# Performance work log

Hardware: AMD Instinct MI355X
Metric: run time of the kernel (lower is better)

## Reference

```python
import jax, jax.numpy as jnp
import numpy as np

DIM = 512
QK_DIM = 128
HIDDEN = 1024


def setup_inputs() -> dict:
    key = jax.random.key(0)
    ks = jax.random.split(key, 8)
    b, n = 4, 4096
    x = jax.random.normal(ks[0], (b, n, DIM), dtype=jnp.float32)
    # nn.Linear(dim, hidden*2)
    w_hidden = jax.random.normal(ks[1], (DIM, 2 * HIDDEN), dtype=jnp.float32) / np.sqrt(DIM)
    b_hidden = jnp.zeros((2 * HIDDEN,), dtype=jnp.float32)
    # nn.Linear(dim, qk_dim, bias=False)
    w_qk = jax.random.normal(ks[2], (DIM, QK_DIM), dtype=jnp.float32) / np.sqrt(DIM)
    # OffsetScale params (gamma init 1, beta init 0; randomize slightly for a nontrivial test)
    q_gamma = 1.0 + 0.02 * jax.random.normal(ks[3], (QK_DIM,), dtype=jnp.float32)
    q_beta = 0.02 * jax.random.normal(ks[4], (QK_DIM,), dtype=jnp.float32)
    k_gamma = 1.0 + 0.02 * jax.random.normal(ks[5], (QK_DIM,), dtype=jnp.float32)
    k_beta = 0.02 * jax.random.normal(ks[6], (QK_DIM,), dtype=jnp.float32)
    # nn.Linear(hidden, dim)
    w_out = jax.random.normal(ks[7], (HIDDEN, DIM), dtype=jnp.float32) / np.sqrt(HIDDEN)
    b_out = jnp.zeros((DIM,), dtype=jnp.float32)
    return {
        "x": x,
        "w_hidden": w_hidden, "b_hidden": b_hidden,
        "w_qk": w_qk,
        "q_gamma": q_gamma, "q_beta": q_beta,
        "k_gamma": k_gamma, "k_beta": k_beta,
        "w_out": w_out, "b_out": b_out,
    }


def reference(x, w_hidden, b_hidden, w_qk, q_gamma, q_beta, k_gamma, k_beta, w_out, b_out):
    scale = QK_DIM ** -0.5
    # to_hidden -> chunk into v, gate (NOTE: source applies no activation here)
    hid = jnp.einsum('bnd,dh->bnh', x, w_hidden) + b_hidden  # [b, n, 2*hidden]
    v, gate = jnp.split(hid, 2, axis=-1)                     # each [b, n, hidden]
    qk = jnp.einsum('bnd,de->bne', x, w_qk)                  # [b, n, qk_dim]
    q = qk * q_gamma + q_beta
    k = qk * k_gamma + k_beta
    sim = jnp.einsum('bid,bjd->bij', q, k) * scale           # [b, n, n]
    attn = jnp.square(jax.nn.relu(sim))                      # ReLU^2, no softmax
    out = jnp.einsum('bij,bjh->bih', attn, v)                # [b, n, hidden]
    out = out * gate
    out = jnp.einsum('bnh,hd->bnd', out, w_out) + b_out      # [b, n, dim]
    return out + x  # add_residual=True
```

## Files before the change

### kernel.cpp

```cpp
#include <hip/hip_runtime.h>
#include <hip/hip_bf16.h>

typedef __attribute__((ext_vector_type(8))) short bf16x8;
typedef __attribute__((ext_vector_type(4))) float f32x4;
typedef unsigned short u16;

__device__ __forceinline__ u16 f2b(float f) {
  __hip_bfloat16 h = __float2bfloat16(f);
  return __builtin_bit_cast(unsigned short, h);
}
__device__ __forceinline__ float b2f(u16 u) {
  __hip_bfloat16 h = __builtin_bit_cast(__hip_bfloat16, u);
  return __bfloat162float(h);
}

#define BAR() __builtin_amdgcn_s_barrier()
#define LGKM0() do { asm volatile("s_waitcnt lgkmcnt(0)" ::: "memory"); __builtin_amdgcn_sched_barrier(0); } while (0)
#define LGKM4() do { asm volatile("s_waitcnt lgkmcnt(4)" ::: "memory"); __builtin_amdgcn_sched_barrier(0); } while (0)
#define LGKM8() do { asm volatile("s_waitcnt lgkmcnt(8)" ::: "memory"); __builtin_amdgcn_sched_barrier(0); } while (0)
#define VMCNT4() asm volatile("s_waitcnt vmcnt(4)" ::: "memory")
#define VMCNT2() asm volatile("s_waitcnt vmcnt(2)" ::: "memory")
#define VMCNT0() asm volatile("s_waitcnt vmcnt(0)" ::: "memory")

#define EPI_HID 0
#define EPI_QK 1
#define EPI_PV 3
#define EPI_OUT 4

__device__ __forceinline__ void stage_tile(char* sbase, const char* gbase, int ld_bytes, int tid) {
#pragma unroll
  for (int i = 0; i < 4; ++i) {
    int o = (i * 256 + tid) * 16;
    int row = o >> 7;
    int cb = o & 127;
    int scb = cb ^ ((row & 7) << 4);
    const char* src = gbase + (long)row * ld_bytes + scb;
    __builtin_amdgcn_global_load_lds((const __attribute__((address_space(1))) void*)src,
                                     (__attribute__((address_space(3))) void*)(sbase + o),
                                     16, 0, 0);
  }
}

template <int EPI>
__global__ __launch_bounds__(256, 2) void gemm_tn(
    const char* Ab, const char* Bb, long sAbat, long sBbat,
    int lda_b, int ldb_b, int nkt,
    u16* o0, u16* o1,
    const float* a0, const float* a1, const float* a2, const float* a3,
    float* fout, const float* xres) {
  __shared__ __align__(16) char lds[32768];
  char* sA = lds;
  char* sB = lds + 16384;
  const int tid = threadIdx.x;
  const int lane = tid & 63;
  const int wave = tid >> 6;
  const int wm = wave >> 1, wn = wave & 1;
  const int l16 = lane & 15, lq = lane >> 4;
  const int bat = blockIdx.z;
  const int row0 = blockIdx.y * 128;
  const int col0 = blockIdx.x * 128;

  const char* Abase = Ab + (long)bat * sAbat + (long)row0 * lda_b;
  const char* Bbase = Bb + (long)bat * sBbat + (long)col0 * ldb_b;

  f32x4 acc[4][4];
#pragma unroll
  for (int i = 0; i < 4; ++i)
#pragma unroll
    for (int j = 0; j < 4; ++j) acc[i][j] = (f32x4){0.f, 0.f, 0.f, 0.f};

  for (int kt = 0; kt < nkt; ++kt) {
    stage_tile(sA, Abase + (long)kt * 128, lda_b, tid);
    stage_tile(sB, Bbase + (long)kt * 128, ldb_b, tid);
    __syncthreads();
#pragma unroll
    for (int kk = 0; kk < 2; ++kk) {
      bf16x8 af[4], bfr[4];
#pragma unroll
      for (int mf = 0; mf < 4; ++mf) {
        int r = wm * 64 + mf * 16 + l16;
        int kb = kk * 64 + lq * 16;
        af[mf] = *(const bf16x8*)(sA + r * 128 + (kb ^ ((r & 7) << 4)));
      }
#pragma unroll
      for (int nf = 0; nf < 4; ++nf) {
        int r = wn * 64 + nf * 16 + l16;
        int kb = kk * 64 + lq * 16;
        bfr[nf] = *(const bf16x8*)(sB + r * 128 + (kb ^ ((r & 7) << 4)));
      }
#pragma unroll
      for (int mf = 0; mf < 4; ++mf)
#pragma unroll
        for (int nf = 0; nf < 4; ++nf)
          acc[mf][nf] = __builtin_amdgcn_mfma_f32_16x16x32_bf16(af[mf], bfr[nf], acc[mf][nf], 0, 0, 0);
    }
    __syncthreads();
  }

#pragma unroll
  for (int mf = 0; mf < 4; ++mf) {
#pragma unroll
    for (int nf = 0; nf < 4; ++nf) {
      const int row = row0 + wm * 64 + mf * 16 + lq * 4;
      const int col = col0 + wn * 64 + nf * 16 + l16;
      f32x4 v = acc[mf][nf];
      if constexpr (EPI == EPI_QK) {
        float qg = a0[col], qbt = a1[col], kg = a2[col], kbt = a3[col];
#pragma unroll
        for (int i = 0; i < 4; ++i) {
          float t = v[i];
          o0[(size_t)(row + i) * 128 + col] = f2b(t * qg + qbt);
          o1[(size_t)(row + i) * 128 + col] = f2b(t * kg + kbt);
        }
      } else if constexpr (EPI == EPI_OUT) {
        float bias = a0[col];
#pragma unroll
        for (int i = 0; i < 4; ++i)
          fout[(size_t)(row + i) * 512 + col] = v[i] + bias + xres[(size_t)(row + i) * 512 + col];
      }
    }
  }
}

__device__ __forceinline__ void stage_half(char* sbase, const char* gbase, long ld, int tid) {
#pragma unroll
  for (int i = 0; i < 2; ++i) {
    int o = (i * 512 + tid) * 16;
    int row = o >> 7;
    int cb = o & 127;
    int scb = cb ^ ((row & 7) << 4);
    const char* src = gbase + (long)row * ld + scb;
    __builtin_amdgcn_global_load_lds((const __attribute__((address_space(1))) void*)src,
                                     (__attribute__((address_space(3))) void*)(sbase + o),
                                     16, 0, 0);
  }
}

template <int EPI>
__global__ __launch_bounds__(512, 1) void gemm256(
    const char* Ab, const char* Bb, long sAbat, long sBbat,
    long lda, long ldb, int nkt, int nx,
    u16* o0, u16* o1,
    const float* a0, float* fout, const float* xres) {
  extern __shared__ __align__(16) char lds[];
  const int tid = threadIdx.x;
  const int lane = tid & 63;
  const int wave = tid >> 6;
  const int wm = wave >> 2;
  const int wn = wave & 3;
  const int l16 = lane & 15, lq = lane >> 4;
  const int bat = blockIdx.y;

  const int nwg = gridDim.x;
  const int qq = nwg >> 3;
  const int fid = blockIdx.x;
  const int swz = (fid & 7) * qq + (fid >> 3);
  const int row0 = (swz / nx) * 256;
  const int col0 = (swz % nx) * 256;

  const char* gA = Ab + (long)bat * sAbat + (long)row0 * lda;
  const char* gB = Bb + (long)bat * sBbat + (long)col0 * ldb;

  f32x4 acc[8][4];
#pragma unroll
  for (int i = 0; i < 8; ++i)
#pragma unroll
    for (int j = 0; j < 4; ++j) acc[i][j] = (f32x4){0.f, 0.f, 0.f, 0.f};

  const int kmask = (l16 & 7) << 4;
  const int kb0 = (lq * 16) ^ kmask;
  const int kb1 = (64 + lq * 16) ^ kmask;
  const int rB = (wn & 1) * 64;

  stage_half(lds + 32768, gB, ldb, tid);
  stage_half(lds + 32768 + 16384, gB + 128 * ldb, ldb, tid);
  stage_half(lds, gA, lda, tid);
  stage_half(lds + 16384, gA + 128 * lda, lda, tid);
  if (nkt > 1) {
    stage_half(lds + 65536 + 32768, gB + 128, ldb, tid);
    stage_half(lds + 65536 + 32768 + 16384, gB + 128 * ldb + 128, ldb, tid);
    VMCNT4();
  } else {
    VMCNT0();
  }
  BAR();

  bf16x8 af0[4], af1[4], afp0[4], afp1[4], bfr0[4], bfr1[4];
  {
    const char* myA = lds + wm * 16384;
    const char* myB = lds + 32768 + (wn >> 1) * 16384;
#pragma unroll
    for (int nf = 0; nf < 4; ++nf)
      bfr0[nf] = *(const bf16x8*)(myB + (rB + nf * 16 + l16) * 128 + kb0);
#pragma unroll
    for (int mf = 0; mf < 4; ++mf)
      af0[mf] = *(const bf16x8*)(myA + (mf * 16 + l16) * 128 + kb0);
  }

  for (int t = 0; t < nkt; ++t) {
    const char* bufc = lds + (t & 1) * 65536;
    const char* bufn = lds + ((t + 1) & 1) * 65536;
    const char* myA = bufc + wm * 16384;
    const char* myB = bufc + 32768 + (wn >> 1) * 16384;
    const char* nA = bufn + wm * 16384;
    const char* nB = bufn + 32768 + (wn >> 1) * 16384;
    char* stA = (char*)bufn;
    char* stB = (char*)bufc + 32768;
    const bool sA_ok = (t + 1) < nkt;
    const bool sB_ok = (t + 2) < nkt;

#pragma unroll
    for (int nf = 0; nf < 4; ++nf)
      bfr1[nf] = *(const bf16x8*)(myB + (rB + nf * 16 + l16) * 128 + kb1);
#pragma unroll
    for (int mf = 0; mf < 4; ++mf)
      af1[mf] = *(const bf16x8*)(myA + (mf * 16 + l16) * 128 + kb1);
    if (sA_ok) stage_half(stA, gA + (long)(t + 1) * 128, lda, tid);
    LGKM8();
    __builtin_amdgcn_s_setprio(1);
#pragma unroll
    for (int mf = 0; mf < 4; ++mf)
#pragma unroll
      for (int nf = 0; nf < 4; ++nf)
        acc[mf][nf] = __builtin_amdgcn_mfma_f32_16x16x32_bf16(af0[mf], bfr0[nf], acc[mf][nf], 0, 0, 0);
    __builtin_amdgcn_s_setprio(0);

#pragma unroll
    for (int mf = 0; mf < 4; ++mf)
      afp0[mf] = *(const bf16x8*)(myA + (64 + mf * 16 + l16) * 128 + kb0);
    if (sA_ok) stage_half(stA + 16384, gA + 128 * lda + (long)(t + 1) * 128, lda, tid);
    LGKM4();
    __builtin_amdgcn_s_setprio(1);
#pragma unroll
    for (int mf = 0; mf < 4; ++mf)
#pragma unroll
      for (int nf = 0; nf < 4; ++nf)
        acc[mf][nf] = __builtin_amdgcn_mfma_f32_16x16x32_bf16(af1[mf], bfr1[nf], acc[mf][nf], 0, 0, 0);
    __builtin_amdgcn_s_setprio(0);
    BAR();

#pragma unroll
    for (int mf = 0; mf < 4; ++mf)
      afp1[mf] = *(const bf16x8*)(myA + (64 + mf * 16 + l16) * 128 + kb1);
    if (sB_ok) stage_half(stB, gB + (long)(t + 2) * 128, ldb, tid);
    LGKM4();
    __builtin_amdgcn_s_setprio(1);
#pragma unroll
    for (int mf = 0; mf < 4; ++mf)
#pragma unroll
      for (int nf = 0; nf < 4; ++nf)
        acc[4 + mf][nf] = __builtin_amdgcn_mfma_f32_16x16x32_bf16(afp0[mf], bfr0[nf], acc[4 + mf][nf], 0, 0, 0);
    __builtin_amdgcn_s_setprio(0);
    if (sA_ok) {
      if (sB_ok) { VMCNT2(); } else { VMCNT0(); }
      BAR();
    }

    if (sA_ok) {
#pragma unroll
      for (int nf = 0; nf < 4; ++nf)
        bfr0[nf] = *(const bf16x8*)(nB + (rB + nf * 16 + l16) * 128 + kb0);
#pragma unroll
      for (int mf = 0; mf < 4; ++mf)
        af0[mf] = *(const bf16x8*)(nA + (mf * 16 + l16) * 128 + kb0);
    }
    if (sB_ok) stage_half(stB + 16384, gB + 128 * ldb + (long)(t + 2) * 128, ldb, tid);
    if (sA_ok) { LGKM8(); } else { LGKM0(); }
    __builtin_amdgcn_s_setprio(1);
#pragma unroll
    for (int mf = 0; mf < 4; ++mf)
#pragma unroll
      for (int nf = 0; nf < 4; ++nf)
        acc[4 + mf][nf] = __builtin_amdgcn_mfma_f32_16x16x32_bf16(afp1[mf], bfr1[nf], acc[4 + mf][nf], 0, 0, 0);
    __builtin_amdgcn_s_setprio(0);
    BAR();
  }

#pragma unroll
  for (int mi = 0; mi < 8; ++mi) {
#pragma unroll
    for (int ni = 0; ni < 4; ++ni) {
      const int row = row0 + wm * 128 + mi * 16 + lq * 4;
      const int col = col0 + wn * 64 + ni * 16 + l16;
      f32x4 v = acc[mi][ni];
      if constexpr (EPI == EPI_HID) {
        float bias = a0[col];
        u16* dst = (col < 1024) ? (o0 + (size_t)col * 16384 + row)
                                : (o1 + (size_t)(col - 1024) * 16384 + row);
        *(ushort4*)dst = make_ushort4(f2b(v.x + bias), f2b(v.y + bias), f2b(v.z + bias), f2b(v.w + bias));
      } else if constexpr (EPI == EPI_PV) {
        const u16* gt = o1 + (size_t)col * 16384 + (size_t)bat * 4096 + row;
        ushort4 g = *(const ushort4*)gt;
        u16* dst = o0 + (size_t)bat * 4096 * 1024;
        dst[(size_t)(row + 0) * 1024 + col] = f2b(v.x * b2f(g.x));
        dst[(size_t)(row + 1) * 1024 + col] = f2b(v.y * b2f(g.y));
        dst[(size_t)(row + 2) * 1024 + col] = f2b(v.z * b2f(g.z));
        dst[(size_t)(row + 3) * 1024 + col] = f2b(v.w * b2f(g.w));
      }
    }
  }
}

__device__ __forceinline__ void stage256(char* s, const char* g, int tid) {
#pragma unroll
  for (int i = 0; i < 8; ++i) {
    int o = (i * 512 + tid) * 16;
    int row = o >> 8;
    int cb = o & 255;
    int scb = cb ^ ((row & 7) << 4);
    __builtin_amdgcn_global_load_lds((const __attribute__((address_space(1))) void*)(g + (long)row * 256 + scb),
                                     (__attribute__((address_space(3))) void*)(s + o), 16, 0, 0);
  }
}

__global__ __launch_bounds__(512, 1) void attn_lean(
    const char* Kb, const char* Qb, u16* o0, int nx) {
  extern __shared__ __align__(16) char lds[];
  const int tid = threadIdx.x;
  const int lane = tid & 63;
  const int wave = tid >> 6;
  const int wm = wave >> 2;
  const int wn = wave & 3;
  const int l16 = lane & 15, lq = lane >> 4;
  const int bat = blockIdx.y;

  const int nwg = gridDim.x;
  const int qq = nwg >> 3;
  const int fid = blockIdx.x;
  const int swz = (fid & 7) * qq + (fid >> 3);
  const int row0 = (swz / nx) * 256;
  const int col0 = (swz % nx) * 256;

  const char* gA = Kb + (size_t)bat * 4096 * 256 + (size_t)row0 * 256;
  const char* gB = Qb + (size_t)bat * 4096 * 256 + (size_t)col0 * 256;

  stage256(lds, gA, tid);
  stage256(lds + 65536, gB, tid);
  VMCNT0();
  BAR();

  const char* myA = lds + wm * 32768;
  const char* myB = lds + 65536 + (wn >> 1) * 32768;
  const int rB = (wn & 1) * 64;
  const int kmask = (l16 & 7) << 4;

  f32x4 acc[8][4];
#pragma unroll
  for (int i = 0; i < 8; ++i)
#pragma unroll
    for (int j = 0; j < 4; ++j) acc[i][j] = (f32x4){0.f, 0.f, 0.f, 0.f};

  bf16x8 aC[8], bC[4], aN[8], bN[4];

#define LOADK(A, B, kk)                                                        \
  do {                                                                         \
    const int kb_ = ((kk) * 64 + lq * 16) ^ kmask;                             \
    _Pragma("unroll") for (int mf = 0; mf < 8; ++mf)                           \
        A[mf] = *(const bf16x8*)(myA + (mf * 16 + l16) * 256 + kb_);           \
    _Pragma("unroll") for (int nf = 0; nf < 4; ++nf)                           \
        B[nf] = *(const bf16x8*)(myB + (rB + nf * 16 + l16) * 256 + kb_);      \
  } while (0)
#define MMK(A, B)                                                              \
  do {                                                                         \
    _Pragma("unroll") for (int mf = 0; mf < 8; ++mf)                           \
        _Pragma("unroll") for (int nf = 0; nf < 4; ++nf)                       \
            acc[mf][nf] =                                                      \
        __builtin_amdgcn_mfma_f32_16x16x32_bf16(A[mf], B[nf], acc[mf][nf], 0, 0, 0); \
  } while (0)

  LOADK(aC, bC, 0);
  LOADK(aN, bN, 1);
  MMK(aC, bC);
  LOADK(aC, bC, 2);
  MMK(aN, bN);
  LOADK(aN, bN, 3);
  MMK(aC, bC);
  MMK(aN, bN);
#undef LOADK
#undef MMK

  const float scale = 0.088388347648318447f;
  u16* dst = o0 + (size_t)bat * 4096 * 4096;
#pragma unroll
  for (int mi = 0; mi < 8; ++mi) {
#pragma unroll
    for (int ni = 0; ni < 4; ++ni) {
      const int row = row0 + wm * 128 + mi * 16 + lq * 4;
      const int col = col0 + wn * 64 + ni * 16 + l16;
      f32x4 v = acc[mi][ni];
      float t0 = v.x * scale; t0 = t0 > 0.f ? t0 * t0 : 0.f;
      float t1 = v.y * scale; t1 = t1 > 0.f ? t1 * t1 : 0.f;
      float t2 = v.z * scale; t2 = t2 > 0.f ? t2 * t2 : 0.f;
      float t3 = v.w * scale; t3 = t3 > 0.f ? t3 * t3 : 0.f;
      *(ushort4*)(dst + (size_t)col * 4096 + row) =
          make_ushort4(f2b(t0), f2b(t1), f2b(t2), f2b(t3));
    }
  }
}

__global__ void conv_b(const float* in, u16* out, int n) {
  int i = (blockIdx.x * blockDim.x + threadIdx.x) * 4;
  if (i >= n) return;
  float4 f = *(const float4*)(in + i);
  *(ushort4*)(out + i) = make_ushort4(f2b(f.x), f2b(f.y), f2b(f.z), f2b(f.w));
}

__global__ void transpose_lds(const float* in, u16* out, int R, int C) {
  __shared__ float t[32][33];
  const int tx = threadIdx.x & 31, ty = threadIdx.x >> 5;
  const int c0 = blockIdx.x * 32, r0 = blockIdx.y * 32;
#pragma unroll
  for (int i = 0; i < 32; i += 8)
    t[ty + i][tx] = in[(size_t)(r0 + ty + i) * C + c0 + tx];
  __syncthreads();
#pragma unroll
  for (int i = 0; i < 32; i += 8)
    out[(size_t)(c0 + ty + i) * R + r0 + tx] = f2b(t[tx][ty + i]);
}

extern "C" void kernel_launch(void* const* d_in, const int* in_sizes, int n_in,
                              void* d_out, int out_size, void* d_ws, size_t ws_size,
                              hipStream_t stream) {
  const float* x = (const float*)d_in[0];
  const float* w_hidden = (const float*)d_in[1];
  const float* b_hidden = (const float*)d_in[2];
  const float* w_qk = (const float*)d_in[3];
  const float* q_gamma = (const float*)d_in[4];
  const float* q_beta = (const float*)d_in[5];
  const float* k_gamma = (const float*)d_in[6];
  const float* k_beta = (const float*)d_in[7];
  const float* w_out = (const float*)d_in[8];
  const float* b_out = (const float*)d_in[9];
  float* out = (float*)d_out;

  char* ws = (char*)d_ws;
  size_t off = 0;
  auto alloc = [&](size_t bytes) { char* p = ws + off; off += (bytes + 255) & ~255ull; return p; };
  u16* xb     = (u16*)alloc(16384ull * 512 * 2);
  u16* wh_t   = (u16*)alloc(2048ull * 512 * 2);
  u16* wqk_t  = (u16*)alloc(128ull * 512 * 2);
  u16* wout_t = (u16*)alloc(512ull * 1024 * 2);
  u16* v_t    = (u16*)alloc(1024ull * 16384 * 2);
  u16* g_t    = (u16*)alloc(1024ull * 16384 * 2);
  u16* qb_a   = (u16*)alloc(16384ull * 128 * 2);
  u16* kb_a   = (u16*)alloc(16384ull * 128 * 2);
  u16* attnb  = (u16*)alloc(4ull * 4096 * 4096 * 2);
  u16* out1b  = (u16*)alloc(16384ull * 1024 * 2);

  (void)hipFuncSetAttribute((const void*)gemm256<EPI_HID>, hipFuncAttributeMaxDynamicSharedMemorySize, 131072);
  (void)hipFuncSetAttribute((const void*)gemm256<EPI_PV>, hipFuncAttributeMaxDynamicSharedMemorySize, 131072);
  (void)hipFuncSetAttribute((const void*)attn_lean, hipFuncAttributeMaxDynamicSharedMemorySize, 131072);

  conv_b<<<(16384 * 512 / 4 + 255) / 256, 256, 0, stream>>>(x, xb, 16384 * 512);
  transpose_lds<<<dim3(2048 / 32, 512 / 32), 256, 0, stream>>>(w_hidden, wh_t, 512, 2048);
  transpose_lds<<<dim3(128 / 32, 512 / 32), 256, 0, stream>>>(w_qk, wqk_t, 512, 128);
  transpose_lds<<<dim3(512 / 32, 1024 / 32), 256, 0, stream>>>(w_out, wout_t, 1024, 512);

  gemm256<EPI_HID><<<dim3(512, 1), 512, 131072, stream>>>(
      (const char*)xb, (const char*)wh_t, 0, 0, 1024, 1024, 8, 8,
      v_t, g_t, b_hidden, nullptr, nullptr);
  gemm_tn<EPI_QK><<<dim3(1, 128, 1), 256, 0, stream>>>(
      (const char*)xb, (const char*)wqk_t, 0, 0, 1024, 1024, 8,
      qb_a, kb_a, q_gamma, q_beta, k_gamma, k_beta, nullptr, nullptr);
  attn_lean<<<dim3(256, 4), 512, 131072, stream>>>(
      (const char*)kb_a, (const char*)qb_a, attnb, 16);
  gemm256<EPI_PV><<<dim3(64, 4), 512, 131072, stream>>>(
      (const char*)attnb, (const char*)v_t, 4096ll * 8192, 8192, 8192, 32768, 64, 4,
      out1b, g_t, nullptr, nullptr, nullptr);
  gemm_tn<EPI_OUT><<<dim3(4, 128, 1), 256, 0, stream>>>(
      (const char*)out1b, (const char*)wout_t, 0, 0, 2048, 2048, 16,
      nullptr, nullptr, b_out, nullptr, nullptr, nullptr, out, x);
}
```

Baseline: 314.7 us.

## Replace PV GEMM with 1024-thread 16-wave kernel using smaller per-wave tiles

```diff
diff --git a/kernel.cpp b/kernel.cpp
--- a/kernel.cpp
+++ b/kernel.cpp
@@ -288,15 +288,147 @@
         u16* dst = (col < 1024) ? (o0 + (size_t)col * 16384 + row)
                                 : (o1 + (size_t)(col - 1024) * 16384 + row);
         *(ushort4*)dst = make_ushort4(f2b(v.x + bias), f2b(v.y + bias), f2b(v.z + bias), f2b(v.w + bias));
-      } else if constexpr (EPI == EPI_PV) {
-        const u16* gt = o1 + (size_t)col * 16384 + (size_t)bat * 4096 + row;
-        ushort4 g = *(const ushort4*)gt;
-        u16* dst = o0 + (size_t)bat * 4096 * 1024;
-        dst[(size_t)(row + 0) * 1024 + col] = f2b(v.x * b2f(g.x));
-        dst[(size_t)(row + 1) * 1024 + col] = f2b(v.y * b2f(g.y));
-        dst[(size_t)(row + 2) * 1024 + col] = f2b(v.z * b2f(g.z));
-        dst[(size_t)(row + 3) * 1024 + col] = f2b(v.w * b2f(g.w));
       }
+    }
+  }
+}
+
+__device__ __forceinline__ void stage1k(char* s, const char* g, long ld, int tid) {
+  int o = tid * 16;
+  int row = o >> 7;
+  int scb = (o & 127) ^ ((row & 7) << 4);
+  __builtin_amdgcn_global_load_lds((const __attribute__((address_space(1))) void*)(g + (long)row * ld + scb),
+                                   (__attribute__((address_space(3))) void*)(s + o), 16, 0, 0);
+}
+
+__global__ __launch_bounds__(1024, 1) void gemm1k_pv(
+    const char* Ab, const char* Bb, long sAbat, long sBbat,
+    long lda, long ldb, int nkt, int nx,
+    u16* o0, const u16* g_t) {
+  extern __shared__ __align__(16) char lds[];
+  const int tid = threadIdx.x;
+  const int lane = tid & 63;
+  const int wave = tid >> 6;
+  const int wm = wave >> 2;
+  const int wn = wave & 3;
+  const int l16 = lane & 15, lq = lane >> 4;
+  const int bat = blockIdx.y;
+
+  const int nwg = gridDim.x;
+  const int qq = nwg >> 3;
+  const int fid = blockIdx.x;
+  const int swz = (fid & 7) * qq + (fid >> 3);
+  const int row0 = (swz / nx) * 256;
+  const int col0 = (swz % nx) * 256;
+
+  const char* gA = Ab + (long)bat * sAbat + (long)row0 * lda;
+  const char* gB = Bb + (long)bat * sBbat + (long)col0 * ldb;
+
+  f32x4 acc[4][4];
+#pragma unroll
+  for (int i = 0; i < 4; ++i)
+#pragma unroll
+    for (int j = 0; j < 4; ++j) acc[i][j] = (f32x4){0.f, 0.f, 0.f, 0.f};
+
+  const int kmask = (l16 & 7) << 4;
+  const int kb0 = (lq * 16) ^ kmask;
+  const int kb1 = (64 + lq * 16) ^ kmask;
+  const int rA = (wm & 1) * 64;
+  const int rB = (wn & 1) * 64;
+
+  stage1k(lds + 32768, gB, ldb, tid);
+  stage1k(lds + 32768 + 16384, gB + 128 * ldb, ldb, tid);
+  stage1k(lds, gA, lda, tid);
+  stage1k(lds + 16384, gA + 128 * lda, lda, tid);
+  if (nkt > 1) {
+    stage1k(lds + 65536 + 32768, gB + 128, ldb, tid);
+    stage1k(lds + 65536 + 32768 + 16384, gB + 128 * ldb + 128, ldb, tid);
+    VMCNT2();
+  } else {
+    VMCNT0();
+  }
+  BAR();
+
+  bf16x8 a[4], b[4];
+  {
+    const char* myA = lds + (wm >> 1) * 16384;
+    const char* myB = lds + 32768 + (wn >> 1) * 16384;
+#pragma unroll
+    for (int mi = 0; mi < 4; ++mi)
+      a[mi] = *(const bf16x8*)(myA + (rA + mi * 16 + l16) * 128 + kb0);
+#pragma unroll
+    for (int ni = 0; ni < 4; ++ni)
+      b[ni] = *(const bf16x8*)(myB + (rB + ni * 16 + l16) * 128 + kb0);
+  }
+
+  for (int t = 0; t < nkt; ++t) {
+    char* bufc = lds + (t & 1) * 65536;
+    char* bufn = lds + ((t + 1) & 1) * 65536;
+    const char* myA = bufc + (wm >> 1) * 16384;
+    const char* myB = bufc + 32768 + (wn >> 1) * 16384;
+    const bool sA = (t + 1) < nkt;
+    const bool sB = (t + 2) < nkt;
+
+    LGKM0();
+    __builtin_amdgcn_s_setprio(1);
+#pragma unroll
+    for (int mi = 0; mi < 4; ++mi)
+#pragma unroll
+      for (int ni = 0; ni < 4; ++ni)
+        acc[mi][ni] = __builtin_amdgcn_mfma_f32_16x16x32_bf16(a[mi], b[ni], acc[mi][ni], 0, 0, 0);
+    __builtin_amdgcn_s_setprio(0);
+#pragma unroll
+    for (int mi = 0; mi < 4; ++mi)
+      a[mi] = *(const bf16x8*)(myA + (rA + mi * 16 + l16) * 128 + kb1);
+#pragma unroll
+    for (int ni = 0; ni < 4; ++ni)
+      b[ni] = *(const bf16x8*)(myB + (rB + ni * 16 + l16) * 128 + kb1);
+    if (sA) {
+      stage1k(bufn, gA + (long)(t + 1) * 128, lda, tid);
+      stage1k(bufn + 16384, gA + 128 * lda + (long)(t + 1) * 128, lda, tid);
+    }
+
+    LGKM0();
+    __builtin_amdgcn_s_setprio(1);
+#pragma unroll
+    for (int mi = 0; mi < 4; ++mi)
+#pragma unroll
+      for (int ni = 0; ni < 4; ++ni)
+        acc[mi][ni] = __builtin_amdgcn_mfma_f32_16x16x32_bf16(a[mi], b[ni], acc[mi][ni], 0, 0, 0);
+    __builtin_amdgcn_s_setprio(0);
+    BAR();
+    if (sB) {
+      stage1k(bufc + 32768, gB + (long)(t + 2) * 128, ldb, tid);
+      stage1k(bufc + 32768 + 16384, gB + 128 * ldb + (long)(t + 2) * 128, ldb, tid);
+    }
+    if (sA) {
+      if (sB) { VMCNT2(); } else { VMCNT0(); }
+      BAR();
+      const char* nA = bufn + (wm >> 1) * 16384;
+      const char* nB = bufn + 32768 + (wn >> 1) * 16384;
+#pragma unroll
+      for (int mi = 0; mi < 4; ++mi)
+        a[mi] = *(const bf16x8*)(nA + (rA + mi * 16 + l16) * 128 + kb0);
+#pragma unroll
+      for (int ni = 0; ni < 4; ++ni)
+        b[ni] = *(const bf16x8*)(nB + (rB + ni * 16 + l16) * 128 + kb0);
+    }
+  }
+
+#pragma unroll
+  for (int mi = 0; mi < 4; ++mi) {
+#pragma unroll
+    for (int ni = 0; ni < 4; ++ni) {
+      const int row = row0 + wm * 64 + mi * 16 + lq * 4;
+      const int col = col0 + wn * 64 + ni * 16 + l16;
+      f32x4 v = acc[mi][ni];
+      const u16* gp = g_t + (size_t)col * 16384 + (size_t)bat * 4096 + row;
+      ushort4 g = *(const ushort4*)gp;
+      u16* dst = o0 + (size_t)bat * 4096 * 1024;
+      dst[(size_t)(row + 0) * 1024 + col] = f2b(v.x * b2f(g.x));
+      dst[(size_t)(row + 1) * 1024 + col] = f2b(v.y * b2f(g.y));
+      dst[(size_t)(row + 2) * 1024 + col] = f2b(v.z * b2f(g.z));
+      dst[(size_t)(row + 3) * 1024 + col] = f2b(v.w * b2f(g.w));
     }
   }
 }
@@ -448,7 +580,7 @@
   u16* out1b  = (u16*)alloc(16384ull * 1024 * 2);
 
   (void)hipFuncSetAttribute((const void*)gemm256<EPI_HID>, hipFuncAttributeMaxDynamicSharedMemorySize, 131072);
-  (void)hipFuncSetAttribute((const void*)gemm256<EPI_PV>, hipFuncAttributeMaxDynamicSharedMemorySize, 131072);
+  (void)hipFuncSetAttribute((const void*)gemm1k_pv, hipFuncAttributeMaxDynamicSharedMemorySize, 131072);
   (void)hipFuncSetAttribute((const void*)attn_lean, hipFuncAttributeMaxDynamicSharedMemorySize, 131072);
 
   conv_b<<<(16384 * 512 / 4 + 255) / 256, 256, 0, stream>>>(x, xb, 16384 * 512);
@@ -464,9 +596,9 @@
       qb_a, kb_a, q_gamma, q_beta, k_gamma, k_beta, nullptr, nullptr);
   attn_lean<<<dim3(256, 4), 512, 131072, stream>>>(
       (const char*)kb_a, (const char*)qb_a, attnb, 16);
-  gemm256<EPI_PV><<<dim3(64, 4), 512, 131072, stream>>>(
+  gemm1k_pv<<<dim3(64, 4), 1024, 131072, stream>>>(
       (const char*)attnb, (const char*)v_t, 4096ll * 8192, 8192, 8192, 32768, 64, 4,
-      out1b, g_t, nullptr, nullptr, nullptr);
+      out1b, g_t);
   gemm_tn<EPI_OUT><<<dim3(4, 128, 1), 256, 0, stream>>>(
       (const char*)out1b, (const char*)wout_t, 0, 0, 2048, 2048, 16,
       nullptr, nullptr, b_out, nullptr, nullptr, nullptr, out, x);
```

After: 321.0 us. 1.02x slower.
